# Kernel optimization log

Measured on AMD Instinct MI355X. Metric: run time of the kernel, lower is better.

## Reference

```python
import jax, jax.numpy as jnp
import numpy as np

EPS = 1e-5

@jax.custom_vjp
def ste_sign(x):
    # Binarize: sign(x); backward is straight-through identity (BNN convention)
    return jnp.sign(x)

def _ste_fwd(x):
    return jnp.sign(x), None

def _ste_bwd(_, g):
    return (g,)

ste_sign.defvjp(_ste_fwd, _ste_bwd)

def bn(y, gamma, beta, mean, var):
    # inference-mode BatchNorm2d over channel axis 1
    inv = gamma * jax.lax.rsqrt(var + EPS)
    return y * inv[None, :, None, None] + (beta - mean * inv)[None, :, None, None]

def setup_inputs() -> dict:
    key = jax.random.key(0)
    ks = jax.random.split(key, 11)
    B, C, H, W = 32, 256, 56, 56
    return {
        "x":  jax.random.normal(ks[0], (B, C, H, W), jnp.float32),
        "w1": jax.random.normal(ks[1], (3 * C, C), jnp.float32),   # 1x1 conv kernel [out,in]
        "w2": jax.random.normal(ks[2], (C, 3 * C), jnp.float32),
        "g1": jax.random.uniform(ks[3], (3 * C,), jnp.float32, 0.5, 1.5),
        "b1": jax.random.normal(ks[4], (3 * C,), jnp.float32),
        "m1": jax.random.normal(ks[5], (3 * C,), jnp.float32),
        "v1": jax.random.uniform(ks[6], (3 * C,), jnp.float32, 0.5, 1.5),
        "g2": jax.random.uniform(ks[7], (C,), jnp.float32, 0.5, 1.5),
        "b2": jax.random.normal(ks[8], (C,), jnp.float32),
        "m2": jax.random.normal(ks[9], (C,), jnp.float32),
        "v2": jax.random.uniform(ks[10], (C,), jnp.float32, 0.5, 1.5),
    }

def reference(x, w1, w2, g1, b1, m1, v1, g2, b2, m2, v2):
    # BinarizeConv2d: binarize input + weight, 1x1 conv == channel GEMM
    y1 = jnp.einsum('oc,bchw->bohw', ste_sign(w1), ste_sign(x))
    y1 = bn(y1, g1, b1, m1, v1)
    y2 = jnp.einsum('oc,bchw->bohw', ste_sign(w2), ste_sign(y1))
    y2 = bn(y2, g2, b2, m2, v2)
    return y2 + x
```

## Files before the change

### kernel.cpp

```cpp
#include <hip/hip_runtime.h>

typedef unsigned long long u64;
typedef int i32x4 __attribute__((ext_vector_type(4)));

#define HW    3136
#define CIN   256
#define CMID  768
#define EPSV  1e-5

__global__ __launch_bounds__(64) void prep_kernel(
    const float* __restrict__ w1, const float* __restrict__ w2,
    const float* __restrict__ g1, const float* __restrict__ b1,
    const float* __restrict__ m1, const float* __restrict__ v1,
    const float* __restrict__ g2, const float* __restrict__ b2,
    const float* __restrict__ m2, const float* __restrict__ v2,
    char* __restrict__ w1b, char* __restrict__ w2b,
    float2* __restrict__ ic1, float2* __restrict__ ic2)
{
  int blk = blockIdx.x, lane = threadIdx.x;
  if (blk < 1536) {
    const float* src = (blk < 768) ? w1 : w2;
    char*        dst = (blk < 768) ? w1b : w2b;
    int idx  = ((blk < 768) ? blk : blk - 768) * 64 + lane;
    int base = idx * 4;
    unsigned d = 0;
    #pragma unroll
    for (int j = 0; j < 4; ++j) {
      float v = src[base + j];
      unsigned s = (v < 0.f) ? 0xFFu : (v > 0.f ? 1u : 0u);
      d |= s << (8 * j);
    }
    *(unsigned*)(dst + base) = d;
  } else {
    int i = (blk - 1536) * 64 + lane;
    if (i < CMID) {
      double inv = (double)g1[i] / sqrt((double)v1[i] + EPSV);
      float2 o; o.x = (float)inv;
      o.y = (float)((double)b1[i] - (double)m1[i] * inv);
      ic1[i] = o;
    } else {
      int j = i - CMID;
      double inv = (double)g2[j] / sqrt((double)v2[j] + EPSV);
      float2 o; o.x = (float)inv;
      o.y = (float)((double)b2[j] - (double)m2[j] * inv);
      ic2[j] = o;
    }
  }
}

__global__ __launch_bounds__(256, 2) void bnn_kernel(
    const float* __restrict__ x,
    const char* __restrict__ w1b, const char* __restrict__ w2b,
    const float2* __restrict__ ic1, const float2* __restrict__ ic2,
    float* __restrict__ out)
{
  __shared__ __align__(16) char sBx[64 * 256];
  __shared__ __align__(16) char sY[64 * 768];

  int t    = threadIdx.x;
  int w    = t >> 6;
  int lane = t & 63;
  int l15  = lane & 15;
  int g4   = lane >> 4;
  int swz  = l15 << 4;

  int px0 = blockIdx.x * 64;
  int b   = px0 / HW;
  int hw0 = px0 - b * HW;
  const float* xb = x   + (size_t)b * (CIN * HW) + hw0;
  float*       ob = out + (size_t)b * (CIN * HW) + hw0;

  {
    const float* xp = xb + lane + (size_t)(w << 6) * HW;
    int rowbase = lane * 256 + (w << 6);
    int pswz    = (lane & 15) << 4;
    #pragma unroll
    for (int j = 0; j < 4; ++j) {
      unsigned d[4];
      #pragma unroll
      for (int q = 0; q < 4; ++q) {
        unsigned dv = 0;
        #pragma unroll
        for (int bb = 0; bb < 4; ++bb) {
          int c = j * 16 + q * 4 + bb;
          unsigned u = __float_as_uint(xp[(size_t)c * HW]);
          unsigned s = ((u + u) == 0u) ? 0u : (((int)u < 0) ? 0xFFu : 1u);
          dv |= s << (8 * bb);
        }
        d[q] = dv;
      }
      i32x4 v; v.x = (int)d[0]; v.y = (int)d[1]; v.z = (int)d[2]; v.w = (int)d[3];
      *(i32x4*)&sBx[(rowbase + j * 16) ^ pswz] = v;
    }
  }
  __syncthreads();

  i32x4 bfa[4][4];
  #pragma unroll
  for (int ks = 0; ks < 4; ++ks) {
    int k0 = ks * 64 + g4 * 16;
    #pragma unroll
    for (int n = 0; n < 4; ++n) {
      int px = n * 16 + l15;
      bfa[ks][n] = *(const i32x4*)&sBx[(px * 256 + k0) ^ swz];
    }
  }

  int wrow = w * 192;
  #pragma unroll 1
  for (int ch = 0; ch < 4; ++ch) {
    int rbase = wrow + ch * 48;
    i32x4 acc[3][4];
    #pragma unroll
    for (int m = 0; m < 3; ++m)
      #pragma unroll
      for (int n = 0; n < 4; ++n) acc[m][n] = (i32x4)0;

    #pragma unroll
    for (int ks = 0; ks < 4; ++ks) {
      int k0 = ks * 64 + g4 * 16;
      i32x4 af[3];
      #pragma unroll
      for (int m = 0; m < 3; ++m) {
        int row = rbase + m * 16 + l15;
        af[m] = *(const i32x4*)&w1b[(size_t)row * 256 + k0];
      }
      #pragma unroll
      for (int m = 0; m < 3; ++m)
        #pragma unroll
        for (int n = 0; n < 4; ++n)
          acc[m][n] = __builtin_amdgcn_mfma_i32_16x16x64_i8(
              af[m], bfa[ks][n], acc[m][n], 0, 0, 0);
    }

    #pragma unroll
    for (int m = 0; m < 3; ++m) {
      int r0 = rbase + m * 16 + g4 * 4;
      float2 c0 = ic1[r0], c1 = ic1[r0 + 1], c2 = ic1[r0 + 2], c3 = ic1[r0 + 3];
      #pragma unroll
      for (int n = 0; n < 4; ++n) {
        int px = n * 16 + l15;
        float y0 = fmaf((float)acc[m][n].x, c0.x, c0.y);
        float y1 = fmaf((float)acc[m][n].y, c1.x, c1.y);
        float y2 = fmaf((float)acc[m][n].z, c2.x, c2.y);
        float y3 = fmaf((float)acc[m][n].w, c3.x, c3.y);
        unsigned dv =
            (unsigned)(y0 < 0.f ? 0xFFu : (y0 > 0.f ? 1u : 0u))
          | ((unsigned)(y1 < 0.f ? 0xFFu : (y1 > 0.f ? 1u : 0u)) << 8)
          | ((unsigned)(y2 < 0.f ? 0xFFu : (y2 > 0.f ? 1u : 0u)) << 16)
          | ((unsigned)(y3 < 0.f ? 0xFFu : (y3 > 0.f ? 1u : 0u)) << 24);
        *(unsigned*)&sY[(px * 768 + r0) ^ swz] = dv;
      }
    }
  }
  __syncthreads();

  {
    int rbase = w << 6;
    i32x4 acc[4][4];
    #pragma unroll
    for (int m = 0; m < 4; ++m)
      #pragma unroll
      for (int n = 0; n < 4; ++n) acc[m][n] = (i32x4)0;

    #pragma unroll 4
    for (int ks = 0; ks < 12; ++ks) {
      int k0 = ks * 64 + g4 * 16;
      i32x4 bf[4];
      #pragma unroll
      for (int n = 0; n < 4; ++n) {
        int px = n * 16 + l15;
        bf[n] = *(const i32x4*)&sY[(px * 768 + k0) ^ swz];
      }
      i32x4 af[4];
      #pragma unroll
      for (int m = 0; m < 4; ++m) {
        int row = rbase + m * 16 + l15;
        af[m] = *(const i32x4*)&w2b[(size_t)row * 768 + k0];
      }
      #pragma unroll
      for (int m = 0; m < 4; ++m)
        #pragma unroll
        for (int n = 0; n < 4; ++n)
          acc[m][n] = __builtin_amdgcn_mfma_i32_16x16x64_i8(
              af[m], bf[n], acc[m][n], 0, 0, 0);
    }

    #pragma unroll
    for (int m = 0; m < 4; ++m) {
      int r0 = rbase + m * 16 + g4 * 4;
      float2 c0 = ic2[r0], c1 = ic2[r0 + 1], c2 = ic2[r0 + 2], c3 = ic2[r0 + 3];
      #pragma unroll
      for (int n = 0; n < 4; ++n) {
        int pxo = n * 16 + l15;
        const float* xq = xb + pxo;
        float*       oq = ob + pxo;
        size_t o0 = (size_t)r0 * HW;
        oq[o0]          = fmaf((float)acc[m][n].x, c0.x, c0.y) + xq[o0];
        oq[o0 + HW]     = fmaf((float)acc[m][n].y, c1.x, c1.y) + xq[o0 + HW];
        oq[o0 + 2 * HW] = fmaf((float)acc[m][n].z, c2.x, c2.y) + xq[o0 + 2 * HW];
        oq[o0 + 3 * HW] = fmaf((float)acc[m][n].w, c3.x, c3.y) + xq[o0 + 3 * HW];
      }
    }
  }
}

extern "C" void kernel_launch(void* const* d_in, const int* in_sizes, int n_in,
                              void* d_out, int out_size, void* d_ws, size_t ws_size,
                              hipStream_t stream) {
  const float* x  = (const float*)d_in[0];
  const float* w1 = (const float*)d_in[1];
  const float* w2 = (const float*)d_in[2];
  const float* g1 = (const float*)d_in[3];
  const float* b1 = (const float*)d_in[4];
  const float* m1 = (const float*)d_in[5];
  const float* v1 = (const float*)d_in[6];
  const float* g2 = (const float*)d_in[7];
  const float* b2 = (const float*)d_in[8];
  const float* m2 = (const float*)d_in[9];
  const float* v2 = (const float*)d_in[10];
  float* out = (float*)d_out;

  char*   w1b = (char*)d_ws;
  char*   w2b = w1b + 196608;
  float2* ic1 = (float2*)(w2b + 196608);
  float2* ic2 = ic1 + CMID;

  prep_kernel<<<1552, 64, 0, stream>>>(w1, w2, g1, b1, m1, v1,
                                       g2, b2, m2, v2, w1b, w2b, ic1, ic2);
  bnn_kernel<<<1568, 256, 0, stream>>>(x, w1b, w2b, ic1, ic2, out);
}
```

Baseline: 132.6 us.

## Bit-pack intermediate activations in LDS to raise occupancy to four blocks

```diff
diff --git a/kernel.cpp b/kernel.cpp
--- a/kernel.cpp
+++ b/kernel.cpp
@@ -7,6 +7,24 @@
 #define CIN   256
 #define CMID  768
 #define EPSV  1e-5
+
+__device__ __forceinline__ u64 shfl_xor64(u64 v, int m) {
+  unsigned lo = (unsigned)__shfl_xor((int)(unsigned)v, m);
+  unsigned hi = (unsigned)__shfl_xor((int)(v >> 32), m);
+  return ((u64)hi << 32) | lo;
+}
+
+__device__ __forceinline__ i32x4 unpack16(unsigned bits) {
+  i32x4 r;
+  #pragma unroll
+  for (int q = 0; q < 4; ++q) {
+    unsigned nib    = (bits >> (4 * q)) & 0xFu;
+    unsigned spread = (nib * 0x00204081u) & 0x01010101u;
+    unsigned d      = 0x01010101u ^ ((spread << 8) - (spread << 1));
+    r[q] = (int)d;
+  }
+  return r;
+}
 
 __global__ __launch_bounds__(64) void prep_kernel(
     const float* __restrict__ w1, const float* __restrict__ w2,
@@ -48,14 +66,14 @@
   }
 }
 
-__global__ __launch_bounds__(256, 2) void bnn_kernel(
+__global__ __launch_bounds__(256, 4) void bnn_kernel(
     const float* __restrict__ x,
     const char* __restrict__ w1b, const char* __restrict__ w2b,
     const float2* __restrict__ ic1, const float2* __restrict__ ic2,
     float* __restrict__ out)
 {
   __shared__ __align__(16) char sBx[64 * 256];
-  __shared__ __align__(16) char sY[64 * 768];
+  __shared__ u64 ssy[12][64];
 
   int t    = threadIdx.x;
   int w    = t >> 6;
@@ -95,63 +113,78 @@
   }
   __syncthreads();
 
-  i32x4 bfa[4][4];
-  #pragma unroll
-  for (int ks = 0; ks < 4; ++ks) {
-    int k0 = ks * 64 + g4 * 16;
-    #pragma unroll
-    for (int n = 0; n < 4; ++n) {
-      int px = n * 16 + l15;
-      bfa[ks][n] = *(const i32x4*)&sBx[(px * 256 + k0) ^ swz];
-    }
-  }
-
   int wrow = w * 192;
-  #pragma unroll 1
-  for (int ch = 0; ch < 4; ++ch) {
-    int rbase = wrow + ch * 48;
-    i32x4 acc[3][4];
-    #pragma unroll
-    for (int m = 0; m < 3; ++m)
+  u64 syb[4][3];
+  #pragma unroll
+  for (int n = 0; n < 4; ++n)
+    #pragma unroll
+    for (int j = 0; j < 3; ++j) syb[n][j] = 0ull;
+
+  #pragma unroll
+  for (int ch = 0; ch < 6; ++ch) {
+    i32x4 acc[2][4];
+    #pragma unroll
+    for (int m = 0; m < 2; ++m)
       #pragma unroll
       for (int n = 0; n < 4; ++n) acc[m][n] = (i32x4)0;
 
     #pragma unroll
     for (int ks = 0; ks < 4; ++ks) {
       int k0 = ks * 64 + g4 * 16;
-      i32x4 af[3];
-      #pragma unroll
-      for (int m = 0; m < 3; ++m) {
-        int row = rbase + m * 16 + l15;
-        af[m] = *(const i32x4*)&w1b[(size_t)row * 256 + k0];
-      }
-      #pragma unroll
-      for (int m = 0; m < 3; ++m)
+      i32x4 bf[4];
+      #pragma unroll
+      for (int n = 0; n < 4; ++n)
+        bf[n] = *(const i32x4*)&sBx[((n * 16 + l15) * 256 + k0) ^ swz];
+      i32x4 af[2];
+      #pragma unroll
+      for (int m = 0; m < 2; ++m)
+        af[m] = *(const i32x4*)&w1b[(size_t)(wrow + ch * 32 + m * 16 + l15) * 256 + k0];
+      #pragma unroll
+      for (int m = 0; m < 2; ++m)
         #pragma unroll
         for (int n = 0; n < 4; ++n)
           acc[m][n] = __builtin_amdgcn_mfma_i32_16x16x64_i8(
-              af[m], bfa[ks][n], acc[m][n], 0, 0, 0);
-    }
-
-    #pragma unroll
-    for (int m = 0; m < 3; ++m) {
-      int r0 = rbase + m * 16 + g4 * 4;
+              af[m], bf[n], acc[m][n], 0, 0, 0);
+    }
+
+    #pragma unroll
+    for (int m = 0; m < 2; ++m) {
+      int base = ch * 32 + m * 16;
+      int wd   = base >> 6;
+      int bo   = base & 63;
+      int r0   = wrow + base + g4 * 4;
       float2 c0 = ic1[r0], c1 = ic1[r0 + 1], c2 = ic1[r0 + 2], c3 = ic1[r0 + 3];
       #pragma unroll
       for (int n = 0; n < 4; ++n) {
-        int px = n * 16 + l15;
         float y0 = fmaf((float)acc[m][n].x, c0.x, c0.y);
         float y1 = fmaf((float)acc[m][n].y, c1.x, c1.y);
         float y2 = fmaf((float)acc[m][n].z, c2.x, c2.y);
         float y3 = fmaf((float)acc[m][n].w, c3.x, c3.y);
-        unsigned dv =
-            (unsigned)(y0 < 0.f ? 0xFFu : (y0 > 0.f ? 1u : 0u))
-          | ((unsigned)(y1 < 0.f ? 0xFFu : (y1 > 0.f ? 1u : 0u)) << 8)
-          | ((unsigned)(y2 < 0.f ? 0xFFu : (y2 > 0.f ? 1u : 0u)) << 16)
-          | ((unsigned)(y3 < 0.f ? 0xFFu : (y3 > 0.f ? 1u : 0u)) << 24);
-        *(unsigned*)&sY[(px * 768 + r0) ^ swz] = dv;
-      }
-    }
+        unsigned nib = (y0 < 0.f ? 1u : 0u) | (y1 < 0.f ? 2u : 0u)
+                     | (y2 < 0.f ? 4u : 0u) | (y3 < 0.f ? 8u : 0u);
+        syb[n][wd] |= (u64)nib << (bo + g4 * 4);
+      }
+    }
+  }
+
+  #pragma unroll
+  for (int n = 0; n < 4; ++n)
+    #pragma unroll
+    for (int j = 0; j < 3; ++j) {
+      u64 v = syb[n][j];
+      v |= shfl_xor64(v, 16);
+      v |= shfl_xor64(v, 32);
+      syb[n][j] = v;
+    }
+  if (g4 == 0) {
+    #pragma unroll
+    for (int n = 0; n < 4; ++n) ssy[3 * w + 0][n * 16 + l15] = syb[n][0];
+  } else if (g4 == 1) {
+    #pragma unroll
+    for (int n = 0; n < 4; ++n) ssy[3 * w + 1][n * 16 + l15] = syb[n][1];
+  } else if (g4 == 2) {
+    #pragma unroll
+    for (int n = 0; n < 4; ++n) ssy[3 * w + 2][n * 16 + l15] = syb[n][2];
   }
   __syncthreads();
 
@@ -163,21 +196,20 @@
       #pragma unroll
       for (int n = 0; n < 4; ++n) acc[m][n] = (i32x4)0;
 
-    #pragma unroll 4
+    #pragma unroll
     for (int ks = 0; ks < 12; ++ks) {
       int k0 = ks * 64 + g4 * 16;
       i32x4 bf[4];
       #pragma unroll
       for (int n = 0; n < 4; ++n) {
-        int px = n * 16 + l15;
-        bf[n] = *(const i32x4*)&sY[(px * 768 + k0) ^ swz];
+        u64 wv = ssy[ks][n * 16 + l15];
+        unsigned bits = (unsigned)(wv >> (g4 * 16)) & 0xFFFFu;
+        bf[n] = unpack16(bits);
       }
       i32x4 af[4];
       #pragma unroll
-      for (int m = 0; m < 4; ++m) {
-        int row = rbase + m * 16 + l15;
-        af[m] = *(const i32x4*)&w2b[(size_t)row * 768 + k0];
-      }
+      for (int m = 0; m < 4; ++m)
+        af[m] = *(const i32x4*)&w2b[(size_t)(rbase + m * 16 + l15) * 768 + k0];
       #pragma unroll
       for (int m = 0; m < 4; ++m)
         #pragma unroll
```

New measurement: 175.4 us. +32.3%, slower.
